# Optimization experiments

Hardware: AMD Instinct MI355X
Metric: run time of the kernel (lower is better)

Reference implementation:

```python
import jax, jax.numpy as jnp
import numpy as np
from jax import lax


def setup_inputs() -> dict:
    key = jax.random.key(0)
    k1, k2 = jax.random.split(key)
    B, C_out, C_in, K, H, W = 16, 128, 128, 3, 64, 64
    features = jax.random.normal(k1, (B, C_in, H, W), dtype=jnp.float32)
    dynamic_kernel = jax.random.normal(k2, (B, C_out, C_in, K, K), dtype=jnp.float32)
    return {"features": features, "dynamic_kernel": dynamic_kernel}


def reference(features, dynamic_kernel):
    # Per-sample dynamic conv. unfold+bmm in torch == cross-correlation (conv2d)
    # with the per-sample kernel; we express it as a vmapped implicit-GEMM conv
    # instead of materializing the (C_in*K*K, H*W) unfold buffer.
    padding = 1

    def conv_one(x, w):  # x: (C_in, H, W), w: (C_out, C_in, K, K)
        return lax.conv_general_dilated(
            x[None],                      # (1, C_in, H, W)
            w,
            window_strides=(1, 1),
            padding=[(padding, padding), (padding, padding)],
            dimension_numbers=("NCHW", "OIHW", "NCHW"),
        )[0]                              # (C_out, H, W)

    return jax.vmap(conv_one)(features, dynamic_kernel)  # (B, C_out, H, W)
```

## Files before the change

### kernel.cpp

```cpp
#include <hip/hip_runtime.h>
#include <stdint.h>

#define BATCH 16
#define CIN   128
#define COUT  128
#define IMG_H 64
#define IMG_W 64
#define HW    4096
#define KTOT  1152
#define XH    66
#define XW    66
#define NCQ   16
#define BM    128
#define BN    64
#define BK    64
#define NSTEPS 18
#define ASTEP 8192
#define BSTEP 4096

typedef __attribute__((ext_vector_type(8))) __bf16 bf16x8;
typedef __attribute__((ext_vector_type(4))) float  f32x4;
typedef __attribute__((address_space(1))) const void* gas_p;
typedef __attribute__((address_space(3))) void*       las_p;

static __device__ __forceinline__ unsigned short f2bf(float f) {
  union { float f; uint32_t u; } c; c.f = f;
  uint32_t r = c.u + 0x7fffu + ((c.u >> 16) & 1u);
  return (unsigned short)(r >> 16);
}

static __device__ __forceinline__ void gload_lds16(const unsigned short* g, unsigned short* l) {
  __builtin_amdgcn_global_load_lds((gas_p)g, (las_p)l, 16, 0, 0);
}

__global__ void prep_fused(const float* __restrict__ x, const float* __restrict__ w,
                           unsigned short* __restrict__ wt4, unsigned short* __restrict__ xpad) {
  const int t = threadIdx.x;
  if (blockIdx.x < BATCH * IMG_H) {
    __shared__ uint32_t tile[64 * 68];
    const int b = blockIdx.x >> 6;
    const int h = blockIdx.x & 63;
    const float* xb = x + (size_t)b * CIN * HW + h * IMG_W;
    uint4* xp4 = (uint4*)xpad;

    const int lane16 = t & 15;
    const int g      = t >> 4;
#pragma unroll
    for (int it = 0; it < 4; ++it) {
      const int ci = it * 32 + g * 2;
      const float4 va = *(const float4*)(xb + (size_t)ci * HW + lane16 * 4);
      const float4 vb = *(const float4*)(xb + (size_t)(ci + 1) * HW + lane16 * 4);
      const float av[4] = {va.x, va.y, va.z, va.w};
      const float bv[4] = {vb.x, vb.y, vb.z, vb.w};
#pragma unroll
      for (int cc = 0; cc < 4; ++cc)
        tile[(lane16 * 4 + cc) * 68 + it * 16 + g] =
            (uint32_t)f2bf(av[cc]) | ((uint32_t)f2bf(bv[cc]) << 16);
    }
    __syncthreads();

    const uint32_t rbase = ((uint32_t)b * XH + h + 1) * NCQ;
#pragma unroll
    for (int it = 0; it < 4; ++it) {
      const int o   = it * 256 + t;
      const int cqg = o >> 6;
      const int wc  = o & 63;
      const uint4 v = *(const uint4*)&tile[wc * 68 + cqg * 4];
      xp4[(rbase + cqg) * XW + wc + 1] = v;
    }
    if (t < 32) {
      const int cqg = t & 15;
      const int col = (t >> 4) ? 65 : 0;
      xp4[(rbase + cqg) * XW + col] = make_uint4(0, 0, 0, 0);
    }
    if (h == 0) {
      const uint32_t r0  = (uint32_t)b * XH * NCQ * XW;
      const uint32_t r65 = ((uint32_t)b * XH + 65) * NCQ * XW;
      for (int i = t; i < NCQ * XW; i += 256) {
        xp4[r0 + i]  = make_uint4(0, 0, 0, 0);
        xp4[r65 + i] = make_uint4(0, 0, 0, 0);
      }
    }
  } else {
    const int idx  = blockIdx.x - BATCH * IMG_H;
    const int b    = idx / NSTEPS;
    const int step = idx % NSTEPS;
    const int khkw = step >> 1;
    const int cib  = (step & 1) << 6;
    const float* wb = w + (size_t)b * COUT * KTOT;
    unsigned short* dst = wt4 + ((size_t)b * NSTEPS + step) * ASTEP;
#pragma unroll
    for (int i = 0; i < 4; ++i) {
      const int c  = i * 256 + t;
      const int cq = c >> 7;
      const int co = c & 127;
      const int ci0 = cib + cq * 8;
      const float* src = wb + (size_t)co * KTOT + (size_t)ci0 * 9 + khkw;
      uint32_t p[4];
#pragma unroll
      for (int e = 0; e < 4; ++e)
        p[e] = (uint32_t)f2bf(src[(2 * e) * 9]) | ((uint32_t)f2bf(src[(2 * e + 1) * 9]) << 16);
      *(uint4*)&dst[(size_t)c * 8] = make_uint4(p[0], p[1], p[2], p[3]);
    }
  }
}

__global__ __launch_bounds__(256, 4) void dynconv_gemm(
    const unsigned short* __restrict__ wt4,
    const unsigned short* __restrict__ xpad,
    float* __restrict__ out) {
  __shared__ alignas(16) unsigned short As[ASTEP];
  __shared__ alignas(16) unsigned short Bs[BSTEP];

  const int t    = threadIdx.x;
  const int b    = blockIdx.y;
  const int oh   = blockIdx.x;

  const int lane = t & 63;
  const int wave = t >> 6;
  const int wm   = (wave & 1) << 6;
  const int wn   = (wave >> 1) << 5;
  const int l15  = lane & 15;
  const int quad = lane >> 4;

  const unsigned short* abase = wt4 + (size_t)b * NSTEPS * ASTEP + (size_t)t * 8;
  const unsigned short* xb = xpad + (size_t)b * XH * NCQ * XW * 8;
  const unsigned short* bbase[2];
#pragma unroll
  for (int i = 0; i < 2; ++i)
    bbase[i] = xb + (size_t)(((i * 4 + wave) * XW) + lane) * 8;

  unsigned short* alds[4];
  unsigned short* blds[2];
#pragma unroll
  for (int i = 0; i < 4; ++i) alds[i] = &As[(i * 256 + wave * 64) * 8];
#pragma unroll
  for (int i = 0; i < 2; ++i) blds[i] = &Bs[((i * 4 + wave) * 64) * 8];

  f32x4 acc[4][2] = {};

  for (int step = 0; step < NSTEPS; ++step) {
    const int khkw = step >> 1;
    const int kh   = (khkw * 11) >> 5;
    const int kw   = khkw - kh * 3;
    const size_t boff = ((size_t)((oh + kh) * NCQ + ((step & 1) << 3)) * XW + kw) * 8;
    const unsigned short* astep = abase + (size_t)step * ASTEP;

#pragma unroll
    for (int i = 0; i < 4; ++i) gload_lds16(astep + i * 2048, alds[i]);
#pragma unroll
    for (int i = 0; i < 2; ++i) gload_lds16(bbase[i] + boff, blds[i]);
    __syncthreads();

#pragma unroll
    for (int ks = 0; ks < 2; ++ks) {
      const int cq = ks * 4 + quad;
      bf16x8 af[4], bf[2];
#pragma unroll
      for (int i = 0; i < 4; ++i) af[i] = *(const bf16x8*)&As[(cq * 128 + wm + i * 16 + l15) * 8];
#pragma unroll
      for (int j = 0; j < 2; ++j) bf[j] = *(const bf16x8*)&Bs[(cq * 64 + wn + j * 16 + l15) * 8];
#pragma unroll
      for (int i = 0; i < 4; ++i)
#pragma unroll
        for (int j = 0; j < 2; ++j)
          acc[i][j] = __builtin_amdgcn_mfma_f32_16x16x32_bf16(af[i], bf[j], acc[i][j], 0, 0, 0);
    }
    __syncthreads();
  }

  float* obase = out + (size_t)b * COUT * HW + oh * 64;
#pragma unroll
  for (int i = 0; i < 4; ++i) {
#pragma unroll
    for (int r = 0; r < 4; ++r) {
      const int row = wm + i * 16 + quad * 4 + r;
      float* orow = obase + (size_t)row * HW;
#pragma unroll
      for (int j = 0; j < 2; ++j)
        orow[wn + j * 16 + l15] = acc[i][j][r];
    }
  }
}

__global__ void dynconv_naive(const float* __restrict__ x, const float* __restrict__ w,
                              float* __restrict__ out) {
  const int o   = blockIdx.x * 256 + threadIdx.x;
  const int pix = o & (HW - 1);
  const int co  = (o >> 12) & (COUT - 1);
  const int b   = o >> 19;
  const int oh  = pix >> 6, ow = pix & 63;
  const float* xb = x + (size_t)b * CIN * HW;
  const float* wb = w + ((size_t)b * COUT + co) * CIN * 9;
  float s = 0.f;
  for (int ci = 0; ci < CIN; ++ci) {
    const float* xc = xb + ci * HW;
    const float* wc = wb + ci * 9;
#pragma unroll
    for (int kh = 0; kh < 3; ++kh) {
      const int ih = oh + kh - 1;
      if ((unsigned)ih >= IMG_H) continue;
#pragma unroll
      for (int kw = 0; kw < 3; ++kw) {
        const int iw = ow + kw - 1;
        if ((unsigned)iw >= IMG_W) continue;
        s += xc[ih * IMG_W + iw] * wc[kh * 3 + kw];
      }
    }
  }
  out[o] = s;
}

extern "C" void kernel_launch(void* const* d_in, const int* in_sizes, int n_in,
                              void* d_out, int out_size, void* d_ws, size_t ws_size,
                              hipStream_t stream) {
  const float* x = (const float*)d_in[0];
  const float* w = (const float*)d_in[1];
  float* out = (float*)d_out;

  const size_t wt_bytes = (size_t)BATCH * NSTEPS * ASTEP * sizeof(unsigned short);
  const size_t xp_bytes = (size_t)BATCH * XH * NCQ * XW * 8 * sizeof(unsigned short);

  if (ws_size >= wt_bytes + xp_bytes) {
    unsigned short* wt4  = (unsigned short*)d_ws;
    unsigned short* xpad = (unsigned short*)((char*)d_ws + wt_bytes);
    prep_fused<<<BATCH * IMG_H + BATCH * NSTEPS, 256, 0, stream>>>(x, w, wt4, xpad);
    dim3 grid(IMG_H, BATCH);
    dynconv_gemm<<<grid, 256, 0, stream>>>(wt4, xpad, out);
  } else {
    dynconv_naive<<<(BATCH * COUT * HW) / 256, 256, 0, stream>>>(x, w, out);
  }
}
```

Before: 124.0 us.

## Double-buffer LDS, widen tile to two output rows, and remap blocks per XCD

The GEMM kernel now runs 512-thread blocks, each computing two adjacent output rows (N=128), so every weight tile loaded into LDS serves twice as many pixels. The A and B tiles are double-buffered: the next K-step's global→LDS loads are issued before the MFMA work on the current buffer, so memory latency can overlap with compute. A 1D grid with an XCD-aware mapping keeps blocks of the same batch sample on the same XCD, which should improve L2 reuse of that sample's weights and input. In exchange, each block needs 64KB of LDS and more waves, which lowers how many blocks can reside per CU, and there are half as many blocks overall.

```diff
diff --git a/kernel.cpp b/kernel.cpp
--- a/kernel.cpp
+++ b/kernel.cpp
@@ -11,12 +11,9 @@
 #define XH    66
 #define XW    66
 #define NCQ   16
-#define BM    128
-#define BN    64
-#define BK    64
 #define NSTEPS 18
 #define ASTEP 8192
-#define BSTEP 4096
+#define BSTEP 8192
 
 typedef __attribute__((ext_vector_type(8))) __bf16 bf16x8;
 typedef __attribute__((ext_vector_type(4))) float  f32x4;
@@ -105,16 +102,19 @@
   }
 }
 
-__global__ __launch_bounds__(256, 4) void dynconv_gemm(
+__global__ __launch_bounds__(512, 4) void dynconv_gemm(
     const unsigned short* __restrict__ wt4,
     const unsigned short* __restrict__ xpad,
     float* __restrict__ out) {
-  __shared__ alignas(16) unsigned short As[ASTEP];
-  __shared__ alignas(16) unsigned short Bs[BSTEP];
-
-  const int t    = threadIdx.x;
-  const int b    = blockIdx.y;
-  const int oh   = blockIdx.x;
+  __shared__ alignas(16) unsigned short As[2][ASTEP];
+  __shared__ alignas(16) unsigned short Bs[2][BSTEP];
+
+  const int t   = threadIdx.x;
+  const int bid = blockIdx.x;
+  const int xcd = bid & 7;
+  const int idx = bid >> 3;
+  const int b   = xcd * 2 + (idx >> 5);
+  const int oh0 = (idx & 31) * 2;
 
   const int lane = t & 63;
   const int wave = t >> 6;
@@ -125,57 +125,76 @@
 
   const unsigned short* abase = wt4 + (size_t)b * NSTEPS * ASTEP + (size_t)t * 8;
   const unsigned short* xb = xpad + (size_t)b * XH * NCQ * XW * 8;
-  const unsigned short* bbase[2];
+  const unsigned short* bconst[2];
 #pragma unroll
   for (int i = 0; i < 2; ++i)
-    bbase[i] = xb + (size_t)(((i * 4 + wave) * XW) + lane) * 8;
-
-  unsigned short* alds[4];
-  unsigned short* blds[2];
-#pragma unroll
-  for (int i = 0; i < 4; ++i) alds[i] = &As[(i * 256 + wave * 64) * 8];
-#pragma unroll
-  for (int i = 0; i < 2; ++i) blds[i] = &Bs[((i * 4 + wave) * 64) * 8];
+    bconst[i] = xb + (size_t)((i * NCQ + wave) * XW + lane) * 8;
+
+  unsigned short* alds[2][2];
+  unsigned short* blds[2][2];
+#pragma unroll
+  for (int u = 0; u < 2; ++u) {
+#pragma unroll
+    for (int r = 0; r < 2; ++r) alds[u][r] = &As[u][(r * 512 + wave * 64) * 8];
+#pragma unroll
+    for (int i = 0; i < 2; ++i) blds[u][i] = &Bs[u][(wave * 128 + i * 64) * 8];
+  }
 
   f32x4 acc[4][2] = {};
 
+  {
+    const size_t boff0 = (size_t)(oh0 * NCQ) * XW * 8;
+#pragma unroll
+    for (int r = 0; r < 2; ++r) gload_lds16(abase + r * 4096, alds[0][r]);
+#pragma unroll
+    for (int i = 0; i < 2; ++i) gload_lds16(bconst[i] + boff0, blds[0][i]);
+  }
+  __syncthreads();
+
+#pragma unroll 2
   for (int step = 0; step < NSTEPS; ++step) {
-    const int khkw = step >> 1;
-    const int kh   = (khkw * 11) >> 5;
-    const int kw   = khkw - kh * 3;
-    const size_t boff = ((size_t)((oh + kh) * NCQ + ((step & 1) << 3)) * XW + kw) * 8;
-    const unsigned short* astep = abase + (size_t)step * ASTEP;
-
-#pragma unroll
-    for (int i = 0; i < 4; ++i) gload_lds16(astep + i * 2048, alds[i]);
-#pragma unroll
-    for (int i = 0; i < 2; ++i) gload_lds16(bbase[i] + boff, blds[i]);
-    __syncthreads();
+    const int cur = step & 1;
+
+    if (step + 1 < NSTEPS) {
+      const int s2   = step + 1;
+      const int khkw = s2 >> 1;
+      const int kh   = (khkw * 11) >> 5;
+      const int kw   = khkw - kh * 3;
+      const size_t boff = ((size_t)((oh0 + kh) * NCQ + ((s2 & 1) << 3)) * XW + kw) * 8;
+      const unsigned short* astep = abase + (size_t)s2 * ASTEP;
+#pragma unroll
+      for (int r = 0; r < 2; ++r) gload_lds16(astep + r * 4096, alds[cur ^ 1][r]);
+#pragma unroll
+      for (int i = 0; i < 2; ++i) gload_lds16(bconst[i] + boff, blds[cur ^ 1][i]);
+    }
 
 #pragma unroll
     for (int ks = 0; ks < 2; ++ks) {
       const int cq = ks * 4 + quad;
       bf16x8 af[4], bf[2];
 #pragma unroll
-      for (int i = 0; i < 4; ++i) af[i] = *(const bf16x8*)&As[(cq * 128 + wm + i * 16 + l15) * 8];
-#pragma unroll
-      for (int j = 0; j < 2; ++j) bf[j] = *(const bf16x8*)&Bs[(cq * 64 + wn + j * 16 + l15) * 8];
+      for (int i = 0; i < 4; ++i)
+        af[i] = *(const bf16x8*)&As[cur][(cq * 128 + wm + i * 16 + l15) * 8];
+#pragma unroll
+      for (int j = 0; j < 2; ++j)
+        bf[j] = *(const bf16x8*)&Bs[cur][(cq * 128 + wn + j * 16 + l15) * 8];
 #pragma unroll
       for (int i = 0; i < 4; ++i)
 #pragma unroll
         for (int j = 0; j < 2; ++j)
           acc[i][j] = __builtin_amdgcn_mfma_f32_16x16x32_bf16(af[i], bf[j], acc[i][j], 0, 0, 0);
     }
+
     __syncthreads();
   }
 
-  float* obase = out + (size_t)b * COUT * HW + oh * 64;
+  float* obase = out + (size_t)b * COUT * HW + (size_t)oh0 * IMG_W;
 #pragma unroll
   for (int i = 0; i < 4; ++i) {
 #pragma unroll
     for (int r = 0; r < 4; ++r) {
-      const int row = wm + i * 16 + quad * 4 + r;
-      float* orow = obase + (size_t)row * HW;
+      const int co = wm + i * 16 + quad * 4 + r;
+      float* orow = obase + (size_t)co * HW;
 #pragma unroll
       for (int j = 0; j < 2; ++j)
         orow[wn + j * 16 + l15] = acc[i][j][r];
@@ -225,8 +244,7 @@
     unsigned short* wt4  = (unsigned short*)d_ws;
     unsigned short* xpad = (unsigned short*)((char*)d_ws + wt_bytes);
     prep_fused<<<BATCH * IMG_H + BATCH * NSTEPS, 256, 0, stream>>>(x, w, wt4, xpad);
-    dim3 grid(IMG_H, BATCH);
-    dynconv_gemm<<<grid, 256, 0, stream>>>(wt4, xpad, out);
+    dynconv_gemm<<<512, 512, 0, stream>>>(wt4, xpad, out);
   } else {
     dynconv_naive<<<(BATCH * COUT * HW) / 256, 256, 0, stream>>>(x, w, out);
   }
```

Result: faster. 121.2 us (-2.3%).
